# Optimization experiments

Measured on AMD Instinct MI355X. Metric: run time of the kernel, lower is better.

## Reference

```python
import jax, jax.numpy as jnp
import numpy as np

B, C = 4096, 1          # batch, num_clusters (C forced to 1 by the view in the original)
S = 2048                # sequence_length
AR = 8                  # ar_order
E = 8                   # exogenous_dim
RD = AR + E


def setup_inputs() -> dict:
    key = jax.random.key(0)
    k1, k2, k3 = jax.random.split(key, 3)
    y = jax.random.normal(k1, (B, C, AR + 1), dtype=jnp.float32)
    u = jax.random.normal(k2, (B, C, S + E), dtype=jnp.float32)
    W = jax.random.normal(k3, (C, RD), dtype=jnp.float32) * 0.05
    return {"y": y, "u": u, "W": W}


def reference(y, u, W):
    # Step i (i = 0..S-1, corresponding to t = AR+1+i) reads u[:, :, 1+i : 1+i+E].
    idx = 1 + jnp.arange(S)[:, None] + jnp.arange(E)[None, :]      # [S, E]
    u_win = jnp.transpose(u[:, :, idx], (2, 0, 1, 3))              # [S, B, C, E]

    w = W[0]  # [RD] — valid since num_clusters == 1 (required by original view)

    def step(window, u_t):
        # window: last AR+1 outputs, [B, C, AR+1]; u_t: [B, C, E]
        diffs = window[:, :, 1:] - window[:, :, :-1]               # [B, C, AR]
        reg = jnp.concatenate([diffs, u_t], axis=2)                # [B, C, RD]
        pred = jnp.einsum('bcr,r->bc', reg, w)                     # [B, C]
        new = window[:, :, -1] + pred                              # [B, C]
        new_window = jnp.concatenate([window[:, :, 1:], new[:, :, None]], axis=2)
        return new_window, new

    _, outs = jax.lax.scan(step, y, u_win)                         # outs: [S, B, C]
    out = jnp.concatenate([y, jnp.transpose(outs, (1, 2, 0))], axis=2)  # [B, C, S+AR+1]
    return out
```

## Files before the change

### kernel.cpp

```cpp
#include <hip/hip_runtime.h>

#define B_TOT 4096
#define S_LEN 2048
#define K_CH  64
#define L_CH  32
#define U_ROW (S_LEN + 8)
#define O_ROW (S_LEN + 9)

struct F4s { float a, b, c, d; };

__global__ __launch_bounds__(256) void arix_fused(
    const float* __restrict__ y, const float* __restrict__ u,
    const float* __restrict__ W, float* __restrict__ out)
{
    __shared__ float Msh[6 * 64];
    __shared__ float Csh[6 * 8];
    const int lt = threadIdx.x;
    const int k  = lt & 63;
    const int b  = blockIdx.x * 4 + (lt >> 6);

    float wd[8], wu[8];
#pragma unroll
    for (int j = 0; j < 8; ++j) { wd[j] = W[j]; wu[j] = W[8 + j]; }

    const float* ub = u + (long)b * U_ROW + k * L_CH;
    float ua[L_CH + 8];
    {
        const float4* up = (const float4*)ub;
#pragma unroll
        for (int q = 0; q < (L_CH + 8) / 4; ++q) {
            float4 v = up[q];
            ua[4*q] = v.x; ua[4*q+1] = v.y; ua[4*q+2] = v.z; ua[4*q+3] = v.w;
        }
    }
    const float* yb = y + b * 9;
    float yv[9];
#pragma unroll
    for (int i = 0; i < 9; ++i) yv[i] = yb[i];

    if (lt < 8) {
        float dr[8];
#pragma unroll
        for (int i = 0; i < 8; ++i) dr[i] = (i == lt) ? 1.f : 0.f;
        float xs = 0.f;
        for (int t = 0; t < L_CH; ++t) {
            float acc = wd[0] * dr[0];
#pragma unroll
            for (int i = 1; i < 8; ++i) acc = fmaf(wd[i], dr[i], acc);
#pragma unroll
            for (int i = 0; i < 7; ++i) dr[i] = dr[i + 1];
            dr[7] = acc; xs += acc;
        }
#pragma unroll
        for (int i = 0; i < 8; ++i) Msh[i * 8 + lt] = dr[i];
        Csh[lt] = xs;
    }
    __syncthreads();
    for (int l = 1; l < 6; ++l) {
        const float* Mp = Msh + (l - 1) * 64;
        const float* Cp = Csh + (l - 1) * 8;
        float mv = 0.f, cv = 0.f;
        if (lt < 64) {
            const int i = lt >> 3, j = lt & 7;
            float a = 0.f;
#pragma unroll
            for (int m = 0; m < 8; ++m) a = fmaf(Mp[i * 8 + m], Mp[m * 8 + j], a);
            mv = a;
        }
        if (lt < 8) {
            float a = Cp[lt];
#pragma unroll
            for (int i = 0; i < 8; ++i) a = fmaf(Cp[i], Mp[i * 8 + lt], a);
            cv = a;
        }
        __syncthreads();
        if (lt < 64) Msh[l * 64 + lt] = mv;
        if (lt < 8)  Csh[l * 8 + lt] = cv;
        __syncthreads();
    }

    float dr[8], x = 0.f;
#pragma unroll
    for (int i = 0; i < 8; ++i) dr[i] = 0.f;
#pragma unroll
    for (int s = 0; s < L_CH; ++s) {
        float acc = wu[0] * ua[s + 1];
#pragma unroll
        for (int j = 1; j < 8; ++j) acc = fmaf(wu[j], ua[s + 1 + j], acc);
#pragma unroll
        for (int j = 0; j < 8; ++j) acc = fmaf(wd[j], dr[j], acc);
#pragma unroll
        for (int j = 0; j < 7; ++j) dr[j] = dr[j + 1];
        dr[7] = acc;
        x += acc;
    }

    float s0[8];
#pragma unroll
    for (int i = 0; i < 8; ++i) s0[i] = yv[i + 1] - yv[i];
    const float x0 = yv[8];

    float P[8], Q = x;
#pragma unroll
    for (int i = 0; i < 8; ++i) P[i] = dr[i];

    if (k == 0) {
        float np[8];
#pragma unroll
        for (int i = 0; i < 8; ++i) {
            float a = P[i];
#pragma unroll
            for (int j = 0; j < 8; ++j) a = fmaf(Msh[i * 8 + j], s0[j], a);
            np[i] = a;
        }
        float qa = Q;
#pragma unroll
        for (int j = 0; j < 8; ++j) qa = fmaf(Csh[j], s0[j], qa);
#pragma unroll
        for (int i = 0; i < 8; ++i) P[i] = np[i];
        Q = qa;
    }

#pragma unroll
    for (int l = 0; l < 6; ++l) {
        const int delta = 1 << l;
        float Pl[8], Ql;
#pragma unroll
        for (int i = 0; i < 8; ++i) Pl[i] = __shfl_up(P[i], delta);
        Ql = __shfl_up(Q, delta);
        if (k >= delta) {
            const float* Mp = Msh + l * 64;
            const float* Cp = Csh + l * 8;
            float np[8];
#pragma unroll
            for (int i = 0; i < 8; ++i) {
                float a = P[i];
#pragma unroll
                for (int j = 0; j < 8; ++j) a = fmaf(Mp[i * 8 + j], Pl[j], a);
                np[i] = a;
            }
            float qa = Q + Ql;
#pragma unroll
            for (int j = 0; j < 8; ++j) qa = fmaf(Cp[j], Pl[j], qa);
#pragma unroll
            for (int i = 0; i < 8; ++i) P[i] = np[i];
            Q = qa;
        }
    }

    float Pin[8], Qin;
#pragma unroll
    for (int i = 0; i < 8; ++i) Pin[i] = __shfl_up(P[i], 1);
    Qin = __shfl_up(Q, 1);
    if (k == 0) {
#pragma unroll
        for (int i = 0; i < 8; ++i) Pin[i] = s0[i];
        Qin = 0.f;
    }

#pragma unroll
    for (int i = 0; i < 8; ++i) dr[i] = Pin[i];
    x = x0 + Qin;

    float* ob = out + (long)b * O_ROW + 9 + k * L_CH;
#pragma unroll
    for (int s4 = 0; s4 < L_CH; s4 += 4) {
        float xo[4];
#pragma unroll
        for (int q = 0; q < 4; ++q) {
            const int s = s4 + q;
            float acc = wu[0] * ua[s + 1];
#pragma unroll
            for (int j = 1; j < 8; ++j) acc = fmaf(wu[j], ua[s + 1 + j], acc);
#pragma unroll
            for (int j = 0; j < 8; ++j) acc = fmaf(wd[j], dr[j], acc);
#pragma unroll
            for (int j = 0; j < 7; ++j) dr[j] = dr[j + 1];
            dr[7] = acc;
            x += acc;
            xo[q] = x;
        }
        F4s v = { xo[0], xo[1], xo[2], xo[3] };
        *(F4s*)(ob + s4) = v;
    }

    if (k < 9) out[(long)b * O_ROW + k] = yv[k];
}

extern "C" void kernel_launch(void* const* d_in, const int* in_sizes, int n_in,
                              void* d_out, int out_size, void* d_ws, size_t ws_size,
                              hipStream_t stream) {
    const float* y = (const float*)d_in[0];
    const float* u = (const float*)d_in[1];
    const float* W = (const float*)d_in[2];
    float* out = (float*)d_out;

    arix_fused<<<dim3(B_TOT / 4), dim3(256), 0, stream>>>(y, u, W, out);
}
```

Measured before the change: 99.28 us.

## Stage u loads and output stores through padded LDS for coalesced global access

Each thread previously loaded its own contiguous chunk of u and wrote its own strided output chunk, so global accesses across a wavefront were strided by 128 bytes. Now each wave loads its row of u coalesced into a padded LDS buffer, threads read their windows from LDS, write results back into the same LDS buffer, and the wave then stores the row to global memory coalesced. The local prefix computation is also moved ahead of the transition-matrix setup so it can overlap, and launch bounds request 4 blocks per CU. The cost is about 34KB of LDS per block, which limits occupancy, plus extra LDS traffic.

After: 99.78 us. About the same (+0.5%).

```diff
diff --git a/kernel.cpp b/kernel.cpp
--- a/kernel.cpp
+++ b/kernel.cpp
@@ -4,55 +4,92 @@
 #define S_LEN 2048
 #define K_CH  64
 #define L_CH  32
-#define U_ROW (S_LEN + 8)
-#define O_ROW (S_LEN + 9)
-
-struct F4s { float a, b, c, d; };
-
-__global__ __launch_bounds__(256) void arix_fused(
+#define U_ROW 2056
+#define O_ROW 2057
+#define PROW  2121
+
+__global__ __launch_bounds__(256, 4) void arix_fused(
     const float* __restrict__ y, const float* __restrict__ u,
     const float* __restrict__ W, float* __restrict__ out)
 {
+    __shared__ float ubuf[4][PROW];
     __shared__ float Msh[6 * 64];
     __shared__ float Csh[6 * 8];
     const int lt = threadIdx.x;
     const int k  = lt & 63;
-    const int b  = blockIdx.x * 4 + (lt >> 6);
+    const int w  = lt >> 6;
+    const int b  = blockIdx.x * 4 + w;
 
     float wd[8], wu[8];
 #pragma unroll
     for (int j = 0; j < 8; ++j) { wd[j] = W[j]; wu[j] = W[8 + j]; }
 
-    const float* ub = u + (long)b * U_ROW + k * L_CH;
-    float ua[L_CH + 8];
+    const float4* up = (const float4*)(u + (long)b * U_ROW);
+    float* ub = ubuf[w];
+#pragma unroll
+    for (int r = 0; r < 8; ++r) {
+        float4 v = up[r * 64 + k];
+        const int g = (r * 64 + k) * 4;
+        const int idx = g + (g >> 5);
+        ub[idx] = v.x; ub[idx + 1] = v.y; ub[idx + 2] = v.z; ub[idx + 3] = v.w;
+    }
+    if (k < 2) {
+        float4 v = up[512 + k];
+        const int g = (512 + k) * 4;
+        const int idx = g + (g >> 5);
+        ub[idx] = v.x; ub[idx + 1] = v.y; ub[idx + 2] = v.z; ub[idx + 3] = v.w;
+    }
+
+    const float* yb = y + b * 9;
+    float s0[8], x0;
     {
-        const float4* up = (const float4*)ub;
-#pragma unroll
-        for (int q = 0; q < (L_CH + 8) / 4; ++q) {
-            float4 v = up[q];
-            ua[4*q] = v.x; ua[4*q+1] = v.y; ua[4*q+2] = v.z; ua[4*q+3] = v.w;
-        }
-    }
-    const float* yb = y + b * 9;
-    float yv[9];
-#pragma unroll
-    for (int i = 0; i < 9; ++i) yv[i] = yb[i];
+        float yv[9];
+#pragma unroll
+        for (int i = 0; i < 9; ++i) yv[i] = yb[i];
+        if (k < 9) out[(long)b * O_ROW + k] = yv[k];
+#pragma unroll
+        for (int i = 0; i < 8; ++i) s0[i] = yv[i + 1] - yv[i];
+        x0 = yv[8];
+    }
+
+    float ua[40];
+    {
+        const int base = 33 * k;
+#pragma unroll
+        for (int j = 1; j < 40; ++j) ua[j] = ub[base + j + (j >> 5)];
+    }
+
+    float dr[8], x = 0.f;
+#pragma unroll
+    for (int i = 0; i < 8; ++i) dr[i] = 0.f;
+#pragma unroll
+    for (int s = 0; s < L_CH; ++s) {
+        float acc = wu[0] * ua[s + 1];
+#pragma unroll
+        for (int j = 1; j < 8; ++j) acc = fmaf(wu[j], ua[s + 1 + j], acc);
+#pragma unroll
+        for (int j = 0; j < 8; ++j) acc = fmaf(wd[j], dr[j], acc);
+#pragma unroll
+        for (int j = 0; j < 7; ++j) dr[j] = dr[j + 1];
+        dr[7] = acc;
+        x += acc;
+    }
 
     if (lt < 8) {
-        float dr[8];
-#pragma unroll
-        for (int i = 0; i < 8; ++i) dr[i] = (i == lt) ? 1.f : 0.f;
+        float tr[8];
+#pragma unroll
+        for (int i = 0; i < 8; ++i) tr[i] = (i == lt) ? 1.f : 0.f;
         float xs = 0.f;
         for (int t = 0; t < L_CH; ++t) {
-            float acc = wd[0] * dr[0];
-#pragma unroll
-            for (int i = 1; i < 8; ++i) acc = fmaf(wd[i], dr[i], acc);
-#pragma unroll
-            for (int i = 0; i < 7; ++i) dr[i] = dr[i + 1];
-            dr[7] = acc; xs += acc;
-        }
-#pragma unroll
-        for (int i = 0; i < 8; ++i) Msh[i * 8 + lt] = dr[i];
+            float acc = wd[0] * tr[0];
+#pragma unroll
+            for (int i = 1; i < 8; ++i) acc = fmaf(wd[i], tr[i], acc);
+#pragma unroll
+            for (int i = 0; i < 7; ++i) tr[i] = tr[i + 1];
+            tr[7] = acc; xs += acc;
+        }
+#pragma unroll
+        for (int i = 0; i < 8; ++i) Msh[i * 8 + lt] = tr[i];
         Csh[lt] = xs;
     }
     __syncthreads();
@@ -79,27 +116,6 @@
         __syncthreads();
     }
 
-    float dr[8], x = 0.f;
-#pragma unroll
-    for (int i = 0; i < 8; ++i) dr[i] = 0.f;
-#pragma unroll
-    for (int s = 0; s < L_CH; ++s) {
-        float acc = wu[0] * ua[s + 1];
-#pragma unroll
-        for (int j = 1; j < 8; ++j) acc = fmaf(wu[j], ua[s + 1 + j], acc);
-#pragma unroll
-        for (int j = 0; j < 8; ++j) acc = fmaf(wd[j], dr[j], acc);
-#pragma unroll
-        for (int j = 0; j < 7; ++j) dr[j] = dr[j + 1];
-        dr[7] = acc;
-        x += acc;
-    }
-
-    float s0[8];
-#pragma unroll
-    for (int i = 0; i < 8; ++i) s0[i] = yv[i + 1] - yv[i];
-    const float x0 = yv[8];
-
     float P[8], Q = x;
 #pragma unroll
     for (int i = 0; i < 8; ++i) P[i] = dr[i];
@@ -162,29 +178,30 @@
     for (int i = 0; i < 8; ++i) dr[i] = Pin[i];
     x = x0 + Qin;
 
-    float* ob = out + (long)b * O_ROW + 9 + k * L_CH;
-#pragma unroll
-    for (int s4 = 0; s4 < L_CH; s4 += 4) {
-        float xo[4];
-#pragma unroll
-        for (int q = 0; q < 4; ++q) {
-            const int s = s4 + q;
-            float acc = wu[0] * ua[s + 1];
-#pragma unroll
-            for (int j = 1; j < 8; ++j) acc = fmaf(wu[j], ua[s + 1 + j], acc);
-#pragma unroll
-            for (int j = 0; j < 8; ++j) acc = fmaf(wd[j], dr[j], acc);
-#pragma unroll
-            for (int j = 0; j < 7; ++j) dr[j] = dr[j + 1];
-            dr[7] = acc;
-            x += acc;
-            xo[q] = x;
-        }
-        F4s v = { xo[0], xo[1], xo[2], xo[3] };
-        *(F4s*)(ob + s4) = v;
-    }
-
-    if (k < 9) out[(long)b * O_ROW + k] = yv[k];
+    const int obase = 33 * k;
+#pragma unroll
+    for (int s = 0; s < L_CH; ++s) {
+        float acc = wu[0] * ua[s + 1];
+#pragma unroll
+        for (int j = 1; j < 8; ++j) acc = fmaf(wu[j], ua[s + 1 + j], acc);
+#pragma unroll
+        for (int j = 0; j < 8; ++j) acc = fmaf(wd[j], dr[j], acc);
+#pragma unroll
+        for (int j = 0; j < 7; ++j) dr[j] = dr[j + 1];
+        dr[7] = acc;
+        x += acc;
+        ub[obase + s] = x;
+    }
+
+    const long orow = (long)b * O_ROW;
+#pragma unroll
+    for (int r = 0; r < 33; ++r) {
+        const int p = r * 64 + k;
+        if (p >= 9 && p < O_ROW) {
+            const int g = p - 9;
+            out[orow + p] = ub[g + (g >> 5)];
+        }
+    }
 }
 
 extern "C" void kernel_launch(void* const* d_in, const int* in_sizes, int n_in,
```
